# Kernel tuning notes

Hardware: AMD Instinct MI355X
Metric: run time of the kernel (lower is better)

The kernel has to match this reference:

```python
import jax, jax.numpy as jnp
import numpy as np

B, L, D, E, R, NMOD = 8, 2048, 4096, 4, 8, 7

def setup_inputs() -> dict:
    key = jax.random.key(0)
    ks = jax.random.split(key, 8)
    return {
        "x": jax.random.normal(ks[0], (B, L, D), dtype=jnp.float32) * 0.02,
        "expert_scores": jax.random.uniform(ks[1], (B, E), dtype=jnp.float32),
        "W_base": jax.random.normal(ks[2], (D, D), dtype=jnp.float32) * 0.02,
        "b_base": jnp.zeros((D,), dtype=jnp.float32),
        "gating_W": jax.random.normal(ks[3], (D, D), dtype=jnp.float32) * 0.02,
        "W_r": jax.random.normal(ks[4], (NMOD, D), dtype=jnp.float32) * 0.02,
        "lora_A": jax.random.normal(ks[5], (E, R, D), dtype=jnp.float32) * 0.02,
        "lora_B": jax.random.normal(ks[6], (E, D, R), dtype=jnp.float32) * 0.02,
        "module_idx": 0,
        "k": 2,
    }

def _gate_weights(expert_scores, module_prob, k, dtype):
    # rank experts by their random score (descending); Top-K -> weight 1/K
    order = jnp.argsort(-expert_scores, axis=-1)           # [B, E]
    rank = jnp.argsort(order, axis=-1)                     # [B, E] rank of each expert
    k_lo = max(1, k // 2)
    w_hi = (rank < k).astype(dtype) / k                    # prob > 0.5 branch
    w_lo = (rank < k_lo).astype(dtype) / k_lo              # prob <= 0.5 branch
    return jnp.where((module_prob > 0.5)[:, None], w_hi, w_lo)  # [B, E]

def reference(x, expert_scores, W_base, b_base, gating_W, W_r, lora_A, lora_B, module_idx, k):
    # Pooler: last token representation
    pooled = x[:, -1, :]                                   # [B, D]
    # Router: softmax(g(h) W_r) -> per-module probability
    gated = pooled @ gating_W.T                            # [B, D]
    logits = gated @ W_r.T                                 # [B, NMOD]
    probs = jax.nn.softmax(logits, axis=-1)
    module_prob = probs[:, module_idx]                     # [B]
    gate = _gate_weights(expert_scores, module_prob, k, x.dtype)  # [B, E]
    # Base linear projection
    base = x @ W_base.T + b_base                           # [B, L, D]
    # LoRA experts: sum_e gate[b,e] * (x @ A_e^T) @ B_e^T
    t = jnp.einsum('bli,eri->belr', x, lora_A)             # [B, E, L, R]
    lora = jnp.einsum('belr,eor,be->blo', t, lora_B, gate) # [B, L, D]
    return base + lora
```

## Files before the change

kernel.cpp:

```cpp
#include <hip/hip_runtime.h>
#include <hip/hip_bf16.h>


typedef short short8 __attribute__((ext_vector_type(8)));
typedef float f32x4v __attribute__((ext_vector_type(4)));

#define M_DIM 16384
#define N_DIM 4096
#define K_DIM 4160
#define D_DIM 4096

__device__ __forceinline__ unsigned short f2b(float f) {
  unsigned u = __builtin_bit_cast(unsigned, f);
  return (unsigned short)((u + 0x7FFFu + ((u >> 16) & 1u)) >> 16);
}
__device__ __forceinline__ void async_copy16(void* lds, const void* g) {
  __builtin_amdgcn_global_load_lds(
      (const __attribute__((address_space(1))) void*)g,
      (__attribute__((address_space(3))) void*)lds, 16, 0, 0);
}
__device__ __forceinline__ short8 frag_ld(const short* base, int row, int ks, int hi, int lo) {
  return *(const short8*)(&base[row * 64 + (((ks * 4 + hi) ^ (lo & 7)) * 8)]);
}

__global__ __launch_bounds__(256) void cvt_x_k(const float* __restrict__ x,
                                               short* __restrict__ xa) {
  size_t idx = (size_t)blockIdx.x * 256 + threadIdx.x;
  size_t row = idx / 520;
  int cc = (int)(idx % 520);
  short8 o;
  if (cc < 512) {
    const float* src = x + row * (size_t)D_DIM + (size_t)cc * 8;
    float4 a = *(const float4*)(src);
    float4 b = *(const float4*)(src + 4);
    o[0] = (short)f2b(a.x); o[1] = (short)f2b(a.y);
    o[2] = (short)f2b(a.z); o[3] = (short)f2b(a.w);
    o[4] = (short)f2b(b.x); o[5] = (short)f2b(b.y);
    o[6] = (short)f2b(b.z); o[7] = (short)f2b(b.w);
  } else {
#pragma unroll
    for (int t = 0; t < 8; ++t) o[t] = 0;
  }
  *(short8*)(xa + row * (size_t)K_DIM + (size_t)cc * 8) = o;
}

__global__ __launch_bounds__(256) void cvt_w_k(const float* __restrict__ Wb,
                                               const float* __restrict__ lB,
                                               short* __restrict__ wa) {
  size_t idx = (size_t)blockIdx.x * 256 + threadIdx.x;
  size_t row = idx / 520;
  int cc = (int)(idx % 520);
  short8 o;
  if (cc < 512) {
    const float* src = Wb + row * (size_t)D_DIM + (size_t)cc * 8;
    float4 a = *(const float4*)(src);
    float4 b = *(const float4*)(src + 4);
    o[0] = (short)f2b(a.x); o[1] = (short)f2b(a.y);
    o[2] = (short)f2b(a.z); o[3] = (short)f2b(a.w);
    o[4] = (short)f2b(b.x); o[5] = (short)f2b(b.y);
    o[6] = (short)f2b(b.z); o[7] = (short)f2b(b.w);
  } else if (cc < 516) {
    int e = cc - 512;
    const float* src = lB + (size_t)e * (D_DIM * 8) + row * 8;
    float4 a = *(const float4*)(src);
    float4 b = *(const float4*)(src + 4);
    o[0] = (short)f2b(a.x); o[1] = (short)f2b(a.y);
    o[2] = (short)f2b(a.z); o[3] = (short)f2b(a.w);
    o[4] = (short)f2b(b.x); o[5] = (short)f2b(b.y);
    o[6] = (short)f2b(b.z); o[7] = (short)f2b(b.w);
  } else {
#pragma unroll
    for (int t = 0; t < 8; ++t) o[t] = 0;
  }
  *(short8*)(wa + row * (size_t)K_DIM + (size_t)cc * 8) = o;
}

__global__ __launch_bounds__(256) void cvt_la_k(const float* __restrict__ lA,
                                                short* __restrict__ lAb) {
  size_t i = (size_t)blockIdx.x * 256 + threadIdx.x;
  const float* s = lA + i * 8;
  float4 a = *(const float4*)s;
  float4 b = *(const float4*)(s + 4);
  short8 o;
  o[0] = (short)f2b(a.x); o[1] = (short)f2b(a.y);
  o[2] = (short)f2b(a.z); o[3] = (short)f2b(a.w);
  o[4] = (short)f2b(b.x); o[5] = (short)f2b(b.y);
  o[6] = (short)f2b(b.z); o[7] = (short)f2b(b.w);
  *(short8*)(lAb + i * 8) = o;
}

__global__ __launch_bounds__(256) void gated_k(const float* __restrict__ x,
                                               const float* __restrict__ gW,
                                               float* __restrict__ gated) {
  const int j = blockIdx.x;
  const int tid = threadIdx.x;
  float acc[8];
#pragma unroll
  for (int b = 0; b < 8; ++b) acc[b] = 0.f;
  const float* w = gW + (size_t)j * D_DIM;
  for (int i = tid * 4; i < D_DIM; i += 1024) {
    float4 wv = *(const float4*)(w + i);
#pragma unroll
    for (int b = 0; b < 8; ++b) {
      const float* p = x + ((size_t)b * 2048 + 2047) * D_DIM + i;
      float4 pv = *(const float4*)p;
      acc[b] += wv.x * pv.x + wv.y * pv.y + wv.z * pv.z + wv.w * pv.w;
    }
  }
  __shared__ float red[8][4];
  const int lane = tid & 63, wv_ = tid >> 6;
#pragma unroll
  for (int b = 0; b < 8; ++b) {
    float v = acc[b];
    v += __shfl_down(v, 32); v += __shfl_down(v, 16); v += __shfl_down(v, 8);
    v += __shfl_down(v, 4);  v += __shfl_down(v, 2);  v += __shfl_down(v, 1);
    if (lane == 0) red[b][wv_] = v;
  }
  __syncthreads();
  if (tid < 8)
    gated[(size_t)tid * D_DIM + j] = red[tid][0] + red[tid][1] + red[tid][2] + red[tid][3];
}

__global__ void gate_k(const float* __restrict__ gated, const float* __restrict__ Wr,
                       const float* __restrict__ scores, const int* __restrict__ midx_p,
                       const int* __restrict__ kp, float* __restrict__ gate) {
  const int lane = threadIdx.x;
  float acc[56];
#pragma unroll
  for (int t = 0; t < 56; ++t) acc[t] = 0.f;
  for (int i = lane * 4; i < D_DIM; i += 256) {
    float4 g[8]; float4 w[7];
#pragma unroll
    for (int b = 0; b < 8; ++b) g[b] = *(const float4*)(gated + (size_t)b * D_DIM + i);
#pragma unroll
    for (int m = 0; m < 7; ++m) w[m] = *(const float4*)(Wr + (size_t)m * D_DIM + i);
#pragma unroll
    for (int m = 0; m < 7; ++m)
#pragma unroll
      for (int b = 0; b < 8; ++b)
        acc[m * 8 + b] += w[m].x * g[b].x + w[m].y * g[b].y + w[m].z * g[b].z + w[m].w * g[b].w;
  }
  __shared__ float Ls[56];
#pragma unroll
  for (int t = 0; t < 56; ++t) {
    float v = acc[t];
    v += __shfl_xor(v, 1); v += __shfl_xor(v, 2); v += __shfl_xor(v, 4);
    v += __shfl_xor(v, 8); v += __shfl_xor(v, 16); v += __shfl_xor(v, 32);
    if (lane == t) Ls[t] = v;
  }
  __syncthreads();
  if (lane < 8) {
    const int b = lane;
    float mx = -1e30f;
    for (int m = 0; m < 7; ++m) mx = fmaxf(mx, Ls[m * 8 + b]);
    float s = 0.f;
    for (int m = 0; m < 7; ++m) s += expf(Ls[m * 8 + b] - mx);
    const int mi = midx_p[0];
    const float mp = expf(Ls[mi * 8 + b] - mx) / s;
    int kv = kp[0]; if (kv < 1) kv = 1;
    int klo = kv >> 1; if (klo < 1) klo = 1;
    float sc[4];
#pragma unroll
    for (int e = 0; e < 4; ++e) sc[e] = scores[b * 4 + e];
#pragma unroll
    for (int e = 0; e < 4; ++e) {
      int rank = 0;
#pragma unroll
      for (int e2 = 0; e2 < 4; ++e2)
        rank += (sc[e2] > sc[e] || (sc[e2] == sc[e] && e2 < e)) ? 1 : 0;
      float wv = (mp > 0.5f) ? ((rank < kv) ? 1.0f / (float)kv : 0.f)
                             : ((rank < klo) ? 1.0f / (float)klo : 0.f);
      gate[b * 4 + e] = wv;
    }
  }
}

__global__ __launch_bounds__(256) void lora_t_k(const short* __restrict__ XA,
                                                const short* __restrict__ LAb,
                                                const float* __restrict__ gate,
                                                short* __restrict__ xa_w) {
  __shared__ short As[4096];
  __shared__ short Bs[2048];
  const int tid = threadIdx.x, lane = tid & 63, wave = tid >> 6;
  const int lo = lane & 15, hi = lane >> 4;
  const size_t row0 = (size_t)blockIdx.x * 64;
  const int srow = tid >> 3;
  const int slot = (tid & 7) ^ (srow & 7);
  const short* gA = XA + (row0 + srow) * (size_t)K_DIM + slot * 8;
  const short* gB = LAb + (size_t)srow * D_DIM + slot * 8;
  f32x4v acc[2] = {};

  for (int t = 0; t < 64; ++t) {
    const int kt = t * 64;
    char* la = (char*)As + wave * 1024;
    char* lb = (char*)Bs + wave * 1024;
    async_copy16(la, gA + kt);
    async_copy16(la + 4096, gA + (size_t)32 * K_DIM + kt);
    async_copy16(lb, gB + kt);
    __syncthreads();
    short8 a0 = frag_ld(As, wave * 16 + lo, 0, hi, lo);
    short8 a1 = frag_ld(As, wave * 16 + lo, 1, hi, lo);
    short8 b00 = frag_ld(Bs, lo, 0, hi, lo);
    short8 b01 = frag_ld(Bs, lo, 1, hi, lo);
    short8 b10 = frag_ld(Bs, 16 + lo, 0, hi, lo);
    short8 b11 = frag_ld(Bs, 16 + lo, 1, hi, lo);
    acc[0] = __builtin_amdgcn_mfma_f32_16x16x32_bf16(a0, b00, acc[0], 0, 0, 0);
    acc[0] = __builtin_amdgcn_mfma_f32_16x16x32_bf16(a1, b01, acc[0], 0, 0, 0);
    acc[1] = __builtin_amdgcn_mfma_f32_16x16x32_bf16(a0, b10, acc[1], 0, 0, 0);
    acc[1] = __builtin_amdgcn_mfma_f32_16x16x32_bf16(a1, b11, acc[1], 0, 0, 0);
    __syncthreads();
  }
  const int b = (int)(row0 >> 11);
#pragma unroll
  for (int ni = 0; ni < 2; ++ni) {
    const int col = ni * 16 + lo;
    const float g = gate[b * 4 + (col >> 3)];
#pragma unroll
    for (int j = 0; j < 4; ++j) {
      const size_t r = row0 + wave * 16 + hi * 4 + j;
      xa_w[r * (size_t)K_DIM + 4096 + col] = (short)f2b(acc[ni][j] * g);
    }
  }
}

__global__ __launch_bounds__(512, 2) void gemm_k(const short* __restrict__ A,
                                                 const short* __restrict__ B,
                                                 const float* __restrict__ bias,
                                                 float* __restrict__ C) {
  __shared__ short As[2][16384];
  __shared__ short Bs[2][16384];
  const int tid = threadIdx.x;
  const int lane = tid & 63;
  const int wave = tid >> 6;
  const int wm = wave >> 2;
  const int wn = wave & 3;
  const int lo = lane & 15, hi = lane >> 4;

  const int wg = (blockIdx.x & 7) * 128 + (blockIdx.x >> 3);
  const int brow = wg >> 4;
  const int bcol = wg & 15;

  const int srow = tid >> 3;
  const int slot = (tid & 7) ^ (srow & 7);
  const short* gA = A + (size_t)(brow * 256 + srow) * K_DIM + slot * 8;
  const short* gB = B + (size_t)(bcol * 256 + srow) * K_DIM + slot * 8;

  float bz[4];
#pragma unroll
  for (int ni = 0; ni < 4; ++ni)
    bz[ni] = bias[bcol * 256 + wn * 64 + ni * 16 + lo];

  f32x4v acc[8][4] = {};

#define STAGE(bufi, kt)                                                          \
  {                                                                              \
    char* la_ = (char*)(&As[bufi][0]) + wave * 1024;                             \
    char* lb_ = (char*)(&Bs[bufi][0]) + wave * 1024;                             \
    _Pragma("unroll")                                                            \
    for (int q_ = 0; q_ < 4; ++q_) {                                             \
      async_copy16(la_ + q_ * 8192, gA + (size_t)q_ * 64 * K_DIM + (kt));        \
      async_copy16(lb_ + q_ * 8192, gB + (size_t)q_ * 64 * K_DIM + (kt));        \
    }                                                                            \
  }

#define COMPUTE(bufi)                                                            \
  {                                                                              \
    const short* Ab_ = &As[bufi][0];                                             \
    const short* Bb_ = &Bs[bufi][0];                                             \
    short8 bfr[4][2];                                                            \
    _Pragma("unroll")                                                            \
    for (int ni = 0; ni < 4; ++ni)                                               \
      _Pragma("unroll")                                                          \
      for (int ks = 0; ks < 2; ++ks)                                             \
        bfr[ni][ks] = frag_ld(Bb_, wn * 64 + ni * 16 + lo, ks, hi, lo);          \
    short8 afr[4][2];                                                            \
    _Pragma("unroll")                                                            \
    for (int mi = 0; mi < 4; ++mi)                                               \
      _Pragma("unroll")                                                          \
      for (int ks = 0; ks < 2; ++ks)                                             \
        afr[mi][ks] = frag_ld(Ab_, wm * 128 + mi * 16 + lo, ks, hi, lo);         \
    __builtin_amdgcn_s_setprio(1);                                               \
    _Pragma("unroll")                                                            \
    for (int mi = 0; mi < 4; ++mi)                                               \
      _Pragma("unroll")                                                          \
      for (int ni = 0; ni < 4; ++ni)                                             \
        _Pragma("unroll")                                                        \
        for (int ks = 0; ks < 2; ++ks)                                           \
          acc[mi][ni] = __builtin_amdgcn_mfma_f32_16x16x32_bf16(                 \
              afr[mi][ks], bfr[ni][ks], acc[mi][ni], 0, 0, 0);                   \
    __builtin_amdgcn_s_setprio(0);                                               \
    _Pragma("unroll")                                                            \
    for (int mi = 0; mi < 4; ++mi)                                               \
      _Pragma("unroll")                                                          \
      for (int ks = 0; ks < 2; ++ks)                                             \
        afr[mi][ks] = frag_ld(Ab_, wm * 128 + 64 + mi * 16 + lo, ks, hi, lo);    \
    __builtin_amdgcn_s_setprio(1);                                               \
    _Pragma("unroll")                                                            \
    for (int mi = 0; mi < 4; ++mi)                                               \
      _Pragma("unroll")                                                          \
      for (int ni = 0; ni < 4; ++ni)                                             \
        _Pragma("unroll")                                                        \
        for (int ks = 0; ks < 2; ++ks)                                           \
          acc[mi + 4][ni] = __builtin_amdgcn_mfma_f32_16x16x32_bf16(             \
              afr[mi][ks], bfr[ni][ks], acc[mi + 4][ni], 0, 0, 0);               \
    __builtin_amdgcn_s_setprio(0);                                               \
  }

  STAGE(0, 0);
  for (int t = 0; t < 64; ++t) {
    const int buf = t & 1;
    STAGE(buf ^ 1, (t + 1) * 64);
    asm volatile("s_waitcnt vmcnt(8)" ::: "memory");
    __builtin_amdgcn_s_barrier();
    asm volatile("" ::: "memory");
    COMPUTE(buf);
    asm volatile("" ::: "memory");
    __builtin_amdgcn_s_barrier();
    asm volatile("" ::: "memory");
  }
  asm volatile("s_waitcnt vmcnt(0)" ::: "memory");
  __builtin_amdgcn_s_barrier();
  asm volatile("" ::: "memory");
  COMPUTE(0);

#pragma unroll
  for (int mi = 0; mi < 8; ++mi) {
#pragma unroll
    for (int ni = 0; ni < 4; ++ni) {
      const int r0 = brow * 256 + wm * 128 + mi * 16 + hi * 4;
      const int c0 = bcol * 256 + wn * 64 + ni * 16 + lo;
#pragma unroll
      for (int j = 0; j < 4; ++j)
        C[(size_t)(r0 + j) * N_DIM + c0] = acc[mi][ni][j] + bz[ni];
    }
  }
#undef STAGE
#undef COMPUTE
}

extern "C" void kernel_launch(void* const* d_in, const int* in_sizes, int n_in,
                              void* d_out, int out_size, void* d_ws, size_t ws_size,
                              hipStream_t stream) {
  const float* x      = (const float*)d_in[0];
  const float* scores = (const float*)d_in[1];
  const float* Wb     = (const float*)d_in[2];
  const float* bb     = (const float*)d_in[3];
  const float* gW     = (const float*)d_in[4];
  const float* Wr     = (const float*)d_in[5];
  const float* lA     = (const float*)d_in[6];
  const float* lB     = (const float*)d_in[7];
  const int*   midx   = (const int*)d_in[8];
  const int*   kk     = (const int*)d_in[9];
  float* out = (float*)d_out;

  char* ws = (char*)d_ws;
  short* xa    = (short*)ws;
  short* wa    = (short*)(ws + 136314880u);
  float* gated = (float*)(ws + 136314880u + 34078720u);
  float* gate  = (float*)(ws + 136314880u + 34078720u + 131072u);
  short* lAb   = (short*)(ws + 136314880u + 34078720u + 131072u + 128u);

  cvt_x_k<<<33280, 256, 0, stream>>>(x, xa);
  cvt_w_k<<<8320, 256, 0, stream>>>(Wb, lB, wa);
  cvt_la_k<<<64, 256, 0, stream>>>(lA, lAb);
  gated_k<<<4096, 256, 0, stream>>>(x, gW, gated);
  gate_k<<<1, 64, 0, stream>>>(gated, Wr, scores, midx, kk, gate);
  lora_t_k<<<256, 256, 0, stream>>>(xa, lAb, gate, xa);
  gemm_k<<<1024, 512, 0, stream>>>(xa, wa, bb, out);
}
```

Before: 805.8 us.

## Restructure GEMM main loop into 4-stage pipeline with 32-wide K slices

Replaces the 2-stage double buffer over 64-wide K tiles with a 4-slot ring of 32-wide K slices, prefetching three slices ahead. A and B loads are split and interleaved between the two MFMA halves, and each half gets its own barrier and waitcnt. A new LDS swizzle fits the narrower rows. The intent is deeper latency hiding with finer interleaving of memory and compute, at the cost of more barriers per K step and more complex slot indexing, which risks hazards.

```diff
diff --git a/kernel.cpp b/kernel.cpp
--- a/kernel.cpp
+++ b/kernel.cpp
@@ -9,6 +9,7 @@
 #define N_DIM 4096
 #define K_DIM 4160
 #define D_DIM 4096
+#define NGRP 130
 
 __device__ __forceinline__ unsigned short f2b(float f) {
   unsigned u = __builtin_bit_cast(unsigned, f);
@@ -227,8 +228,8 @@
                                                  const short* __restrict__ B,
                                                  const float* __restrict__ bias,
                                                  float* __restrict__ C) {
-  __shared__ short As[2][16384];
-  __shared__ short Bs[2][16384];
+  __shared__ short As[4][8192];
+  __shared__ short Bs[4][8192];
   const int tid = threadIdx.x;
   const int lane = tid & 63;
   const int wave = tid >> 6;
@@ -240,10 +241,16 @@
   const int brow = wg >> 4;
   const int bcol = wg & 15;
 
-  const int srow = tid >> 3;
-  const int slot = (tid & 7) ^ (srow & 7);
-  const short* gA = A + (size_t)(brow * 256 + srow) * K_DIM + slot * 8;
-  const short* gB = B + (size_t)(bcol * 256 + srow) * K_DIM + slot * 8;
+  const int srow = tid >> 2;
+  const int schunk = (tid & 3) ^ ((tid >> 3) & 3);
+  const short* srcA = A + (size_t)(brow * 256 + srow) * K_DIM + schunk * 8;
+  const short* srcB = B + (size_t)(bcol * 256 + srow) * K_DIM + schunk * 8;
+  char* ldsA0 = (char*)(&As[0][0]) + wave * 1024;
+  char* ldsB0 = (char*)(&Bs[0][0]) + wave * 1024;
+
+  const int csw = (hi ^ ((lo >> 1) & 3)) * 8;
+  const int aro = (wm * 128 + lo) * 32 + csw;
+  const int bro = (wn * 64 + lo) * 32 + csw;
 
   float bz[4];
 #pragma unroll
@@ -252,76 +259,66 @@
 
   f32x4v acc[8][4] = {};
 
-#define STAGE(bufi, kt)                                                          \
-  {                                                                              \
-    char* la_ = (char*)(&As[bufi][0]) + wave * 1024;                             \
-    char* lb_ = (char*)(&Bs[bufi][0]) + wave * 1024;                             \
-    _Pragma("unroll")                                                            \
-    for (int q_ = 0; q_ < 4; ++q_) {                                             \
-      async_copy16(la_ + q_ * 8192, gA + (size_t)q_ * 64 * K_DIM + (kt));        \
-      async_copy16(lb_ + q_ * 8192, gB + (size_t)q_ * 64 * K_DIM + (kt));        \
-    }                                                                            \
-  }
-
-#define COMPUTE(bufi)                                                            \
-  {                                                                              \
-    const short* Ab_ = &As[bufi][0];                                             \
-    const short* Bb_ = &Bs[bufi][0];                                             \
-    short8 bfr[4][2];                                                            \
-    _Pragma("unroll")                                                            \
-    for (int ni = 0; ni < 4; ++ni)                                               \
-      _Pragma("unroll")                                                          \
-      for (int ks = 0; ks < 2; ++ks)                                             \
-        bfr[ni][ks] = frag_ld(Bb_, wn * 64 + ni * 16 + lo, ks, hi, lo);          \
-    short8 afr[4][2];                                                            \
-    _Pragma("unroll")                                                            \
-    for (int mi = 0; mi < 4; ++mi)                                               \
-      _Pragma("unroll")                                                          \
-      for (int ks = 0; ks < 2; ++ks)                                             \
-        afr[mi][ks] = frag_ld(Ab_, wm * 128 + mi * 16 + lo, ks, hi, lo);         \
-    __builtin_amdgcn_s_setprio(1);                                               \
-    _Pragma("unroll")                                                            \
-    for (int mi = 0; mi < 4; ++mi)                                               \
-      _Pragma("unroll")                                                          \
-      for (int ni = 0; ni < 4; ++ni)                                             \
-        _Pragma("unroll")                                                        \
-        for (int ks = 0; ks < 2; ++ks)                                           \
-          acc[mi][ni] = __builtin_amdgcn_mfma_f32_16x16x32_bf16(                 \
-              afr[mi][ks], bfr[ni][ks], acc[mi][ni], 0, 0, 0);                   \
-    __builtin_amdgcn_s_setprio(0);                                               \
-    _Pragma("unroll")                                                            \
-    for (int mi = 0; mi < 4; ++mi)                                               \
-      _Pragma("unroll")                                                          \
-      for (int ks = 0; ks < 2; ++ks)                                             \
-        afr[mi][ks] = frag_ld(Ab_, wm * 128 + 64 + mi * 16 + lo, ks, hi, lo);    \
-    __builtin_amdgcn_s_setprio(1);                                               \
-    _Pragma("unroll")                                                            \
-    for (int mi = 0; mi < 4; ++mi)                                               \
-      _Pragma("unroll")                                                          \
-      for (int ni = 0; ni < 4; ++ni)                                             \
-        _Pragma("unroll")                                                        \
-        for (int ks = 0; ks < 2; ++ks)                                           \
-          acc[mi + 4][ni] = __builtin_amdgcn_mfma_f32_16x16x32_bf16(             \
-              afr[mi][ks], bfr[ni][ks], acc[mi + 4][ni], 0, 0, 0);               \
-    __builtin_amdgcn_s_setprio(0);                                               \
-  }
-
-  STAGE(0, 0);
-  for (int t = 0; t < 64; ++t) {
-    const int buf = t & 1;
-    STAGE(buf ^ 1, (t + 1) * 64);
+#define STAGE_A(koff, ss)                                                      \
+  async_copy16(ldsA0 + (ss) * 16384, srcA + (koff));                           \
+  async_copy16(ldsA0 + (ss) * 16384 + 8192, srcA + (size_t)128 * K_DIM + (koff));
+#define STAGE_B(koff, ss)                                                      \
+  async_copy16(ldsB0 + (ss) * 16384, srcB + (koff));                           \
+  async_copy16(ldsB0 + (ss) * 16384 + 8192, srcB + (size_t)128 * K_DIM + (koff));
+
+  STAGE_A(0, 0);  STAGE_B(0, 0);
+  STAGE_A(32, 1); STAGE_B(32, 1);
+  STAGE_A(64, 2); STAGE_B(64, 2);
+  asm volatile("s_waitcnt vmcnt(8)" ::: "memory");
+  __builtin_amdgcn_s_barrier();
+
+  for (int g = 0; g < NGRP; ++g) {
+    const int slot = g & 3;
+    const int gs = (g <= NGRP - 4) ? (g + 3) : (g - 1);
+    const int ss = gs & 3;
+    const size_t ko = (size_t)gs * 32;
+    const short* Aslot = &As[0][0] + slot * 8192;
+    const short* Bslot = &Bs[0][0] + slot * 8192;
+
+    short8 afr[4], bfr[4];
+#pragma unroll
+    for (int mi = 0; mi < 4; ++mi)
+      afr[mi] = *(const short8*)(&Aslot[aro + mi * 512]);
+#pragma unroll
+    for (int ni = 0; ni < 4; ++ni)
+      bfr[ni] = *(const short8*)(&Bslot[bro + ni * 512]);
+    STAGE_A(ko, ss);
+    __builtin_amdgcn_s_barrier();
+    asm volatile("s_waitcnt lgkmcnt(0)" ::: "memory");
+    __builtin_amdgcn_sched_barrier(0);
+    __builtin_amdgcn_s_setprio(1);
+#pragma unroll
+    for (int mi = 0; mi < 4; ++mi)
+#pragma unroll
+      for (int ni = 0; ni < 4; ++ni)
+        acc[mi][ni] = __builtin_amdgcn_mfma_f32_16x16x32_bf16(afr[mi], bfr[ni], acc[mi][ni], 0, 0, 0);
+    __builtin_amdgcn_s_setprio(0);
+    __builtin_amdgcn_s_barrier();
+
+    short8 afr2[4];
+#pragma unroll
+    for (int mi = 0; mi < 4; ++mi)
+      afr2[mi] = *(const short8*)(&Aslot[aro + 2048 + mi * 512]);
+    STAGE_B(ko, ss);
     asm volatile("s_waitcnt vmcnt(8)" ::: "memory");
     __builtin_amdgcn_s_barrier();
-    asm volatile("" ::: "memory");
-    COMPUTE(buf);
-    asm volatile("" ::: "memory");
+    asm volatile("s_waitcnt lgkmcnt(0)" ::: "memory");
+    __builtin_amdgcn_sched_barrier(0);
+    __builtin_amdgcn_s_setprio(1);
+#pragma unroll
+    for (int mi = 0; mi < 4; ++mi)
+#pragma unroll
+      for (int ni = 0; ni < 4; ++ni)
+        acc[mi + 4][ni] = __builtin_amdgcn_mfma_f32_16x16x32_bf16(afr2[mi], bfr[ni], acc[mi + 4][ni], 0, 0, 0);
+    __builtin_amdgcn_s_setprio(0);
     __builtin_amdgcn_s_barrier();
-    asm volatile("" ::: "memory");
   }
   asm volatile("s_waitcnt vmcnt(0)" ::: "memory");
-  __builtin_amdgcn_s_barrier();
-  asm volatile("" ::: "memory");
-  COMPUTE(0);
 
 #pragma unroll
   for (int mi = 0; mi < 8; ++mi) {
@@ -334,8 +331,8 @@
         C[(size_t)(r0 + j) * N_DIM + c0] = acc[mi][ni][j] + bz[ni];
     }
   }
-#undef STAGE
-#undef COMPUTE
+#undef STAGE_A
+#undef STAGE_B
 }
 
 extern "C" void kernel_launch(void* const* d_in, const int* in_sizes, int n_in,
```

Result: slower. 882.5 us (+9.5%).
